# Optimization experiments

Measured on AMD Instinct MI355X. Metric: run time of the kernel, lower is better.

The kernel has to match this reference:

```python
import jax, jax.numpy as jnp
import numpy as np

B, N, K, H = 4, 1024, 48, 128
E = 128          # edge feature dim; num_in = E + H = 256
FF = 4 * H       # dense feedforward width
EPS = 1e-5
SCALE = 30.0


def gelu(x):
    return jax.nn.gelu(x, approximate=False)


def linear(x, w, b):
    # torch Linear: w is [out, in]
    return x @ w.T + b


def layer_norm(x, g, b):
    mu = jnp.mean(x, axis=-1, keepdims=True)
    var = jnp.var(x, axis=-1, keepdims=True)
    return (x - mu) * jax.lax.rsqrt(var + EPS) * g + b


def gather_nodes(nodes, idx):
    # nodes [B,N,H], idx [B,N,K] -> [B,N,K,H]
    b, n, k = idx.shape
    flat = idx.reshape(b, n * k, 1)
    return jnp.take_along_axis(nodes, flat, axis=1).reshape(b, n, k, -1)


def setup_inputs():
    key = jax.random.key(0)
    ks = jax.random.split(key, 24)
    s = 0.05
    inp = {
        "h_V": jax.random.normal(ks[0], (B, N, H), jnp.float32),
        "h_E": jax.random.normal(ks[1], (B, N, K, E), jnp.float32),
        "E_idx": jax.random.randint(ks[2], (B, N, K), 0, N, jnp.int64),
        "mask_V": jnp.ones((B, N), jnp.float32),
        "mask_attend": jnp.ones((B, N, K), jnp.float32),
        # node-update message MLP (input dim H + E + H = 3H here)
        "W1_w": jax.random.normal(ks[3], (H, H + E + H), jnp.float32) * s,
        "W1_b": jnp.zeros((H,), jnp.float32),
        "W2_w": jax.random.normal(ks[4], (H, H), jnp.float32) * s,
        "W2_b": jnp.zeros((H,), jnp.float32),
        "W3_w": jax.random.normal(ks[5], (H, H), jnp.float32) * s,
        "W3_b": jnp.zeros((H,), jnp.float32),
        # edge-update message MLP
        "W11_w": jax.random.normal(ks[6], (H, H + E + H), jnp.float32) * s,
        "W11_b": jnp.zeros((H,), jnp.float32),
        "W12_w": jax.random.normal(ks[7], (H, H), jnp.float32) * s,
        "W12_b": jnp.zeros((H,), jnp.float32),
        "W13_w": jax.random.normal(ks[8], (H, H), jnp.float32) * s,
        "W13_b": jnp.zeros((H,), jnp.float32),
        # layer norms
        "ln0_g": jnp.ones((H,), jnp.float32), "ln0_b": jnp.zeros((H,), jnp.float32),
        "ln1_g": jnp.ones((H,), jnp.float32), "ln1_b": jnp.zeros((H,), jnp.float32),
        "ln2_g": jnp.ones((H,), jnp.float32), "ln2_b": jnp.zeros((H,), jnp.float32),
        # position-wise feedforward
        "Win_w": jax.random.normal(ks[9], (FF, H), jnp.float32) * s,
        "Win_b": jnp.zeros((FF,), jnp.float32),
        "Wout_w": jax.random.normal(ks[10], (H, FF), jnp.float32) * s,
        "Wout_b": jnp.zeros((H,), jnp.float32),
        # ReZero residual weight (init 0 in the module; nonzero for testing)
        "resweight": jax.random.normal(ks[11], (1,), jnp.float32) * 0.1,
    }
    return inp


def reference(h_V, h_E, E_idx, mask_V, mask_attend,
              W1_w, W1_b, W2_w, W2_b, W3_w, W3_b,
              W11_w, W11_b, W12_w, W12_b, W13_w, W13_b,
              ln0_g, ln0_b, ln1_g, ln1_b, ln2_g, ln2_b,
              Win_w, Win_b, Wout_w, Wout_b, resweight):
    # ---- node update (pre-norm, ReZero-scaled residual), dropout=eval ----
    residual = h_V
    hVn = layer_norm(h_V, ln0_g, ln0_b)
    h_nbr = gather_nodes(hVn, E_idx)                              # [B,N,K,H]
    h_EV = jnp.concatenate(
        [jnp.broadcast_to(hVn[:, :, None, :], (B, N, K, H)), h_E, h_nbr], axis=-1)
    h_message = linear(gelu(linear(gelu(linear(h_EV, W1_w, W1_b)), W2_w, W2_b)), W3_w, W3_b)
    h_message = mask_attend[..., None] * h_message
    dh = jnp.sum(h_message, axis=-2) / SCALE
    h_V = residual + dh * resweight

    # ---- position-wise feedforward ----
    residual = h_V
    hVn = layer_norm(h_V, ln1_g, ln1_b)
    dh = linear(gelu(linear(hVn, Win_w, Win_b)), Wout_w, Wout_b)
    h_V = residual + dh * resweight
    h_V = mask_V[..., None] * h_V

    # ---- edge update (no ReZero scaling on this branch) ----
    residual = h_E
    hEn = layer_norm(h_E, ln2_g, ln2_b)
    h_nbr = gather_nodes(h_V, E_idx)
    h_EV = jnp.concatenate(
        [jnp.broadcast_to(h_V[:, :, None, :], (B, N, K, H)), hEn, h_nbr], axis=-1)
    h_message = linear(gelu(linear(gelu(linear(h_EV, W11_w, W11_b)), W12_w, W12_b)), W13_w, W13_b)
    h_E = residual + h_message

    return h_V, h_E
```

## Files before the change

kernel.cpp:

```cpp
#include <hip/hip_runtime.h>
#include <hip/hip_bf16.h>

#define BB 4
#define NN 1024
#define KK 48
#define HH 128
#define EE 128
#define IN3 384
#define FF 512
#define ST 132

typedef __attribute__((ext_vector_type(8))) short bf16x8;
typedef __attribute__((ext_vector_type(4))) float f32x4;

#define MFMA(a, b, c) __builtin_amdgcn_mfma_f32_16x16x32_bf16((a), (b), (c), 0, 0, 0)

__device__ __forceinline__ float bf2f(ushort u) {
    union { uint i; float f; } v; v.i = ((uint)u) << 16; return v.f;
}
__device__ __forceinline__ uint cvtpk(float a, float b) {
    uint r;
    asm("v_cvt_pk_bf16_f32 %0, %1, %2" : "=v"(r) : "v"(a), "v"(b));
    return r;
}
__device__ __forceinline__ ushort f2bf1(float v) {
    return (ushort)cvtpk(v, v);
}
__device__ __forceinline__ float wsum(float x) {
    #pragma unroll
    for (int o = 32; o; o >>= 1) x += __shfl_xor(x, o, 64);
    return x;
}
__device__ __forceinline__ float gelu_f(float x) {
    float t = x * fmaf(x * x, 0.044715f, 1.0f);
    float a = fminf(t * 2.3022061f, 50.0f);
    float z;
    asm("v_exp_f32 %0, %1" : "=v"(z) : "v"(a));
    float r;
    asm("v_rcp_f32 %0, %1" : "=v"(r) : "v"(z + 1.0f));
    return x * z * r;
}

__global__ __launch_bounds__(256) void k_cvt8(
    const float* __restrict__ s0, const float* __restrict__ s1,
    const float* __restrict__ s2, const float* __restrict__ s3,
    const float* __restrict__ s4, const float* __restrict__ s5,
    const float* __restrict__ s6, const float* __restrict__ s7,
    ushort* __restrict__ d0, ushort* __restrict__ d1,
    ushort* __restrict__ d2, ushort* __restrict__ d3,
    ushort* __restrict__ d4, ushort* __restrict__ d5,
    ushort* __restrict__ d6, ushort* __restrict__ d7) {
    int i = blockIdx.x * 256 + threadIdx.x;
    const float* s; ushort* d; int base;
    if      (i < 12288) { s = s0; d = d0; base = 0; }
    else if (i < 16384) { s = s1; d = d1; base = 12288; }
    else if (i < 20480) { s = s2; d = d2; base = 16384; }
    else if (i < 32768) { s = s3; d = d3; base = 20480; }
    else if (i < 36864) { s = s4; d = d4; base = 32768; }
    else if (i < 40960) { s = s5; d = d5; base = 36864; }
    else if (i < 57344) { s = s6; d = d6; base = 40960; }
    else                { s = s7; d = d7; base = 57344; }
    int j = i - base;
    float4 v = ((const float4*)s)[j];
    uint2 o;
    o.x = cvtpk(v.x, v.y);
    o.y = cvtpk(v.z, v.w);
    ((uint2*)d)[j] = o;
}

__global__ __launch_bounds__(256) void k_ln0(const float* __restrict__ hV,
                                             const float* __restrict__ g,
                                             const float* __restrict__ bta,
                                             ushort* __restrict__ out) {
    int row = blockIdx.x * 4 + (threadIdx.x >> 6);
    int l = threadIdx.x & 63;
    const float* src = hV + (size_t)row * HH;
    float x0 = src[l], x1 = src[l + 64];
    float s = wsum(x0 + x1);
    float q = wsum(x0 * x0 + x1 * x1);
    float mu = s * (1.0f / 128.0f);
    float rstd = rsqrtf(q * (1.0f / 128.0f) - mu * mu + 1e-5f);
    ushort* dst = out + (size_t)row * HH;
    dst[l]      = f2bf1((x0 - mu) * rstd * g[l]      + bta[l]);
    dst[l + 64] = f2bf1((x1 - mu) * rstd * g[l + 64] + bta[l + 64]);
}

__global__ __launch_bounds__(256, 4) void k_node(
    const float* __restrict__ hV, const float* __restrict__ hE,
    const int* __restrict__ Eidx, const float* __restrict__ maskAtt,
    const ushort* __restrict__ W1w, const float* __restrict__ W1b,
    const ushort* __restrict__ W2w, const float* __restrict__ W2b,
    const ushort* __restrict__ W3w, const float* __restrict__ W3b,
    const float* __restrict__ resw,
    const ushort* __restrict__ hVn,
    float* __restrict__ outHVp) {

    __shared__ ushort buf[96 * ST];
    __shared__ float  sMask[96];
    __shared__ float  sCol[256];

    const int t = threadIdx.x;
    const int w = t >> 6;
    const int lane = t & 63;
    const int np = blockIdx.x * 2;
    const int b  = np >> 10;
    const int r16 = lane & 15, g4 = lane >> 4;

    int myidx[6];
    #pragma unroll
    for (int mt = 0; mt < 6; mt++)
        myidx[mt] = Eidx[np * KK + mt * 16 + r16];
    if (t < 96) sMask[t] = maskAtt[np * KK + t];

    f32x4 acc[6][2];
    #pragma unroll
    for (int mt = 0; mt < 6; mt++) {
        acc[mt][0] = (f32x4){0.f, 0.f, 0.f, 0.f};
        acc[mt][1] = (f32x4){0.f, 0.f, 0.f, 0.f};
    }

    const ushort* Wp  = W1w + (w * 32 + r16) * IN3 + g4 * 8;
    const float*  hE0 = hE + (size_t)np * KK * EE;

    #pragma unroll
    for (int kt = 0; kt < 4; kt++) {
        bf16x8 b0 = *(const bf16x8*)(Wp + 128 + kt * 32);
        bf16x8 b1 = *(const bf16x8*)(Wp + 16 * IN3 + 128 + kt * 32);
        #pragma unroll
        for (int mt = 0; mt < 6; mt++) {
            const float* p = hE0 + (size_t)(mt * 16 + r16) * EE + kt * 32 + g4 * 8;
            float4 f0 = *(const float4*)(p);
            float4 f1 = *(const float4*)(p + 4);
            union { uint u[4]; bf16x8 v; } a;
            a.u[0] = cvtpk(f0.x, f0.y); a.u[1] = cvtpk(f0.z, f0.w);
            a.u[2] = cvtpk(f1.x, f1.y); a.u[3] = cvtpk(f1.z, f1.w);
            acc[mt][0] = MFMA(a.v, b0, acc[mt][0]);
            acc[mt][1] = MFMA(a.v, b1, acc[mt][1]);
        }
    }
    {
        const ushort* nb = hVn + (size_t)b * NN * HH + g4 * 8;
        #pragma unroll
        for (int kt = 0; kt < 4; kt++) {
            bf16x8 b0 = *(const bf16x8*)(Wp + 256 + kt * 32);
            bf16x8 b1 = *(const bf16x8*)(Wp + 16 * IN3 + 256 + kt * 32);
            #pragma unroll
            for (int mt = 0; mt < 6; mt++) {
                bf16x8 a = *(const bf16x8*)(nb + (size_t)myidx[mt] * HH + kt * 32);
                acc[mt][0] = MFMA(a, b0, acc[mt][0]);
                acc[mt][1] = MFMA(a, b1, acc[mt][1]);
            }
        }
    }
    {
        const ushort* sp0 = hVn + (size_t)np * HH + g4 * 8;
        const ushort* sp1 = sp0 + HH;
        #pragma unroll
        for (int kt = 0; kt < 4; kt++) {
            bf16x8 a0 = *(const bf16x8*)(sp0 + kt * 32);
            bf16x8 a1 = *(const bf16x8*)(sp1 + kt * 32);
            bf16x8 b0 = *(const bf16x8*)(Wp + kt * 32);
            bf16x8 b1 = *(const bf16x8*)(Wp + 16 * IN3 + kt * 32);
            #pragma unroll
            for (int mt = 0; mt < 6; mt++) {
                bf16x8 a = (mt < 3) ? a0 : a1;
                acc[mt][0] = MFMA(a, b0, acc[mt][0]);
                acc[mt][1] = MFMA(a, b1, acc[mt][1]);
            }
        }
    }
    #pragma unroll
    for (int nn = 0; nn < 2; nn++) {
        int col = w * 32 + nn * 16 + r16;
        float bb = W1b[col];
        #pragma unroll
        for (int mt = 0; mt < 6; mt++)
            #pragma unroll
            for (int r = 0; r < 4; r++)
                buf[(mt * 16 + g4 * 4 + r) * ST + col] = f2bf1(gelu_f(acc[mt][nn][r] + bb));
    }
    __syncthreads();

    f32x4 acc2[6][2];
    #pragma unroll
    for (int mt = 0; mt < 6; mt++) {
        acc2[mt][0] = (f32x4){0.f, 0.f, 0.f, 0.f};
        acc2[mt][1] = (f32x4){0.f, 0.f, 0.f, 0.f};
    }
    {
        const ushort* Wp2 = W2w + (w * 32 + r16) * HH + g4 * 8;
        #pragma unroll
        for (int kt = 0; kt < 4; kt++) {
            bf16x8 b0 = *(const bf16x8*)(Wp2 + kt * 32);
            bf16x8 b1 = *(const bf16x8*)(Wp2 + 16 * HH + kt * 32);
            #pragma unroll
            for (int mt = 0; mt < 6; mt++) {
                bf16x8 a = *(const bf16x8*)&buf[(mt * 16 + r16) * ST + kt * 32 + g4 * 8];
                acc2[mt][0] = MFMA(a, b0, acc2[mt][0]);
                acc2[mt][1] = MFMA(a, b1, acc2[mt][1]);
            }
        }
    }
    __syncthreads();
    #pragma unroll
    for (int nn = 0; nn < 2; nn++) {
        int col = w * 32 + nn * 16 + r16;
        float bb = W2b[col];
        #pragma unroll
        for (int mt = 0; mt < 6; mt++)
            #pragma unroll
            for (int r = 0; r < 4; r++)
                buf[(mt * 16 + g4 * 4 + r) * ST + col] = f2bf1(gelu_f(acc2[mt][nn][r] + bb));
    }
    __syncthreads();

    f32x4 acc3[6][2];
    #pragma unroll
    for (int mt = 0; mt < 6; mt++) {
        acc3[mt][0] = (f32x4){0.f, 0.f, 0.f, 0.f};
        acc3[mt][1] = (f32x4){0.f, 0.f, 0.f, 0.f};
    }
    {
        const ushort* Wp3 = W3w + (w * 32 + r16) * HH + g4 * 8;
        #pragma unroll
        for (int kt = 0; kt < 4; kt++) {
            bf16x8 b0 = *(const bf16x8*)(Wp3 + kt * 32);
            bf16x8 b1 = *(const bf16x8*)(Wp3 + 16 * HH + kt * 32);
            #pragma unroll
            for (int mt = 0; mt < 6; mt++) {
                bf16x8 a = *(const bf16x8*)&buf[(mt * 16 + r16) * ST + kt * 32 + g4 * 8];
                acc3[mt][0] = MFMA(a, b0, acc3[mt][0]);
                acc3[mt][1] = MFMA(a, b1, acc3[mt][1]);
            }
        }
    }
    {
        float b3a = W3b[w * 32 + r16];
        float b3b = W3b[w * 32 + 16 + r16];
        float s0a = 0.f, s0b = 0.f, s1a = 0.f, s1b = 0.f;
        #pragma unroll
        for (int mt = 0; mt < 6; mt++)
            #pragma unroll
            for (int r = 0; r < 4; r++) {
                int row = mt * 16 + g4 * 4 + r;
                float mk = sMask[row];
                float v0 = (acc3[mt][0][r] + b3a) * mk;
                float v1 = (acc3[mt][1][r] + b3b) * mk;
                if (mt < 3) { s0a += v0; s0b += v1; }
                else        { s1a += v0; s1b += v1; }
            }
        s0a += __shfl_xor(s0a, 16, 64); s0a += __shfl_xor(s0a, 32, 64);
        s0b += __shfl_xor(s0b, 16, 64); s0b += __shfl_xor(s0b, 32, 64);
        s1a += __shfl_xor(s1a, 16, 64); s1a += __shfl_xor(s1a, 32, 64);
        s1b += __shfl_xor(s1b, 16, 64); s1b += __shfl_xor(s1b, 32, 64);
        if (g4 == 0) {
            sCol[w * 32 + r16]            = s0a;
            sCol[w * 32 + 16 + r16]       = s0b;
            sCol[128 + w * 32 + r16]      = s1a;
            sCol[128 + w * 32 + 16 + r16] = s1b;
        }
    }
    __syncthreads();

    {
        float rw = resw[0];
        size_t o = (size_t)np * HH + t;
        outHVp[o] = hV[o] + sCol[t] * (1.0f / 30.0f) * rw;
    }
}

__global__ __launch_bounds__(256, 4) void k_ffn(
    const float* __restrict__ maskV,
    const float* __restrict__ ln1g, const float* __restrict__ ln1b,
    const ushort* __restrict__ Winw, const float* __restrict__ Winb,
    const ushort* __restrict__ Woutw, const float* __restrict__ Woutb,
    const float* __restrict__ resw,
    const float* __restrict__ hVp,
    float* __restrict__ outV,
    ushort* __restrict__ hV2b) {

    __shared__ float  sHVp[16 * 132];
    __shared__ ushort sX[16 * 136];
    __shared__ ushort sY[16 * 520];
    __shared__ float  sMk[16];

    const int t = threadIdx.x;
    const int w = t >> 6;
    const int lane = t & 63;
    const int nb = blockIdx.x * 16;
    const int r16 = lane & 15, g4 = lane >> 4;

    #pragma unroll
    for (int i = 0; i < 8; i++) {
        int e = t + i * 256;
        sHVp[(e >> 7) * 132 + (e & 127)] = hVp[(size_t)nb * HH + e];
    }
    if (t < 16) sMk[t] = maskV[nb + t];
    __syncthreads();

    #pragma unroll
    for (int i = 0; i < 4; i++) {
        int row = w * 4 + i;
        float x0 = sHVp[row * 132 + lane], x1 = sHVp[row * 132 + 64 + lane];
        float s = wsum(x0 + x1);
        float q = wsum(x0 * x0 + x1 * x1);
        float mu = s * (1.0f / 128.0f);
        float rstd = rsqrtf(q * (1.0f / 128.0f) - mu * mu + 1e-5f);
        sX[row * 136 + lane]      = f2bf1((x0 - mu) * rstd * ln1g[lane]      + ln1b[lane]);
        sX[row * 136 + 64 + lane] = f2bf1((x1 - mu) * rstd * ln1g[64 + lane] + ln1b[64 + lane]);
    }
    __syncthreads();

    f32x4 acc1[8];
    #pragma unroll
    for (int nn = 0; nn < 8; nn++) acc1[nn] = (f32x4){0.f, 0.f, 0.f, 0.f};
    bf16x8 a1[4];
    #pragma unroll
    for (int kt = 0; kt < 4; kt++)
        a1[kt] = *(const bf16x8*)&sX[r16 * 136 + kt * 32 + g4 * 8];
    #pragma unroll
    for (int nn = 0; nn < 8; nn++) {
        const ushort* Wq = Winw + (w * 128 + nn * 16 + r16) * HH + g4 * 8;
        #pragma unroll
        for (int kt = 0; kt < 4; kt++)
            acc1[nn] = MFMA(a1[kt], *(const bf16x8*)(Wq + kt * 32), acc1[nn]);
    }
    #pragma unroll
    for (int nn = 0; nn < 8; nn++) {
        int col = w * 128 + nn * 16 + r16;
        float bb = Winb[col];
        #pragma unroll
        for (int r = 0; r < 4; r++)
            sY[(g4 * 4 + r) * 520 + col] = f2bf1(gelu_f(acc1[nn][r] + bb));
    }
    __syncthreads();

    f32x4 acc2[2];
    acc2[0] = (f32x4){0.f, 0.f, 0.f, 0.f};
    acc2[1] = (f32x4){0.f, 0.f, 0.f, 0.f};
    {
        const ushort* Wq = Woutw + (w * 32 + r16) * FF + g4 * 8;
        #pragma unroll 4
        for (int kt = 0; kt < 16; kt++) {
            bf16x8 a = *(const bf16x8*)&sY[r16 * 520 + kt * 32 + g4 * 8];
            acc2[0] = MFMA(a, *(const bf16x8*)(Wq + kt * 32), acc2[0]);
            acc2[1] = MFMA(a, *(const bf16x8*)(Wq + 16 * FF + kt * 32), acc2[1]);
        }
    }
    float rw = resw[0];
    #pragma unroll
    for (int nn = 0; nn < 2; nn++) {
        int col = w * 32 + nn * 16 + r16;
        float bb = Woutb[col];
        #pragma unroll
        for (int r = 0; r < 4; r++) {
            int row = g4 * 4 + r;
            float out = sHVp[row * 132 + col] + (acc2[nn][r] + bb) * rw;
            out *= sMk[row];
            outV[(size_t)(nb + row) * HH + col] = out;
            hV2b[(size_t)(nb + row) * HH + col] = f2bf1(out);
        }
    }
}

__global__ __launch_bounds__(512, 4) void k_edge(
    const float* __restrict__ hE, const int* __restrict__ Eidx,
    const ushort* __restrict__ W11w, const float* __restrict__ W11b,
    const ushort* __restrict__ W12w, const float* __restrict__ W12b,
    const ushort* __restrict__ W13w, const float* __restrict__ W13b,
    const float* __restrict__ ln2g, const float* __restrict__ ln2b,
    const ushort* __restrict__ hV2b,
    float* __restrict__ outE) {

    __shared__ ushort buf[96 * ST];
    __shared__ ushort rawE[96 * ST];

    const int t = threadIdx.x;
    const int w = t >> 6;
    const int lane = t & 63;
    const int rg = w >> 2;
    const int cg = w & 3;
    const int np = blockIdx.x * 2;
    const int b  = np >> 10;
    const size_t eb = (size_t)np * KK * EE;
    const int r16 = lane & 15, g4 = lane >> 4;

    int myidx[3];
    #pragma unroll
    for (int mt = 0; mt < 3; mt++)
        myidx[mt] = Eidx[np * KK + rg * 48 + mt * 16 + r16];

    {
        float g0 = ln2g[2 * lane], g1 = ln2g[2 * lane + 1];
        float c0 = ln2b[2 * lane], c1 = ln2b[2 * lane + 1];
        #pragma unroll 3
        for (int i = 0; i < 12; i++) {
            int k = w + i * 8;
            float2 pr = ((const float2*)(hE + eb + (size_t)k * EE))[lane];
            *(uint*)&rawE[k * ST + 2 * lane] = cvtpk(pr.x, pr.y);
            float s = wsum(pr.x + pr.y);
            float q = wsum(pr.x * pr.x + pr.y * pr.y);
            float mu = s * (1.0f / 128.0f);
            float rstd = rsqrtf(q * (1.0f / 128.0f) - mu * mu + 1e-5f);
            uint packed = cvtpk((pr.x - mu) * rstd * g0 + c0, (pr.y - mu) * rstd * g1 + c1);
            *(uint*)&buf[k * ST + 2 * lane] = packed;
        }
    }
    __syncthreads();

    f32x4 acc[3][2];
    #pragma unroll
    for (int mt = 0; mt < 3; mt++) {
        acc[mt][0] = (f32x4){0.f, 0.f, 0.f, 0.f};
        acc[mt][1] = (f32x4){0.f, 0.f, 0.f, 0.f};
    }
    const ushort* Wp = W11w + (cg * 32 + r16) * IN3 + g4 * 8;
    {
        const ushort* nb = hV2b + (size_t)b * NN * HH + g4 * 8;
        #pragma unroll
        for (int kt = 0; kt < 4; kt++) {
            bf16x8 b0 = *(const bf16x8*)(Wp + 256 + kt * 32);
            bf16x8 b1 = *(const bf16x8*)(Wp + 16 * IN3 + 256 + kt * 32);
            #pragma unroll
            for (int mt = 0; mt < 3; mt++) {
                bf16x8 a = *(const bf16x8*)(nb + (size_t)myidx[mt] * HH + kt * 32);
                acc[mt][0] = MFMA(a, b0, acc[mt][0]);
                acc[mt][1] = MFMA(a, b1, acc[mt][1]);
            }
        }
    }
    #pragma unroll
    for (int kt = 0; kt < 4; kt++) {
        bf16x8 b0 = *(const bf16x8*)(Wp + 128 + kt * 32);
        bf16x8 b1 = *(const bf16x8*)(Wp + 16 * IN3 + 128 + kt * 32);
        #pragma unroll
        for (int mt = 0; mt < 3; mt++) {
            bf16x8 a = *(const bf16x8*)&buf[(rg * 48 + mt * 16 + r16) * ST + kt * 32 + g4 * 8];
            acc[mt][0] = MFMA(a, b0, acc[mt][0]);
            acc[mt][1] = MFMA(a, b1, acc[mt][1]);
        }
    }
    {
        const ushort* sp = hV2b + (size_t)(np + rg) * HH + g4 * 8;
        #pragma unroll
        for (int kt = 0; kt < 4; kt++) {
            bf16x8 aself = *(const bf16x8*)(sp + kt * 32);
            bf16x8 b0 = *(const bf16x8*)(Wp + kt * 32);
            bf16x8 b1 = *(const bf16x8*)(Wp + 16 * IN3 + kt * 32);
            #pragma unroll
            for (int mt = 0; mt < 3; mt++) {
                acc[mt][0] = MFMA(aself, b0, acc[mt][0]);
                acc[mt][1] = MFMA(aself, b1, acc[mt][1]);
            }
        }
    }
    __syncthreads();
    #pragma unroll
    for (int nn = 0; nn < 2; nn++) {
        int col = cg * 32 + nn * 16 + r16;
        float bb = W11b[col];
        #pragma unroll
        for (int mt = 0; mt < 3; mt++)
            #pragma unroll
            for (int r = 0; r < 4; r++)
                buf[(rg * 48 + mt * 16 + g4 * 4 + r) * ST + col] = f2bf1(gelu_f(acc[mt][nn][r] + bb));
    }
    __syncthreads();

    f32x4 acc2[3][2];
    #pragma unroll
    for (int mt = 0; mt < 3; mt++) {
        acc2[mt][0] = (f32x4){0.f, 0.f, 0.f, 0.f};
        acc2[mt][1] = (f32x4){0.f, 0.f, 0.f, 0.f};
    }
    {
        const ushort* Wp2 = W12w + (cg * 32 + r16) * HH + g4 * 8;
        #pragma unroll
        for (int kt = 0; kt < 4; kt++) {
            bf16x8 b0 = *(const bf16x8*)(Wp2 + kt * 32);
            bf16x8 b1 = *(const bf16x8*)(Wp2 + 16 * HH + kt * 32);
            #pragma unroll
            for (int mt = 0; mt < 3; mt++) {
                bf16x8 a = *(const bf16x8*)&buf[(rg * 48 + mt * 16 + r16) * ST + kt * 32 + g4 * 8];
                acc2[mt][0] = MFMA(a, b0, acc2[mt][0]);
                acc2[mt][1] = MFMA(a, b1, acc2[mt][1]);
            }
        }
    }
    __syncthreads();
    #pragma unroll
    for (int nn = 0; nn < 2; nn++) {
        int col = cg * 32 + nn * 16 + r16;
        float bb = W12b[col];
        #pragma unroll
        for (int mt = 0; mt < 3; mt++)
            #pragma unroll
            for (int r = 0; r < 4; r++)
                buf[(rg * 48 + mt * 16 + g4 * 4 + r) * ST + col] = f2bf1(gelu_f(acc2[mt][nn][r] + bb));
    }
    __syncthreads();

    f32x4 acc3[3][2];
    #pragma unroll
    for (int mt = 0; mt < 3; mt++) {
        acc3[mt][0] = (f32x4){0.f, 0.f, 0.f, 0.f};
        acc3[mt][1] = (f32x4){0.f, 0.f, 0.f, 0.f};
    }
    {
        const ushort* Wp3 = W13w + (cg * 32 + r16) * HH + g4 * 8;
        #pragma unroll
        for (int kt = 0; kt < 4; kt++) {
            bf16x8 b0 = *(const bf16x8*)(Wp3 + kt * 32);
            bf16x8 b1 = *(const bf16x8*)(Wp3 + 16 * HH + kt * 32);
            #pragma unroll
            for (int mt = 0; mt < 3; mt++) {
                bf16x8 a = *(const bf16x8*)&buf[(rg * 48 + mt * 16 + r16) * ST + kt * 32 + g4 * 8];
                acc3[mt][0] = MFMA(a, b0, acc3[mt][0]);
                acc3[mt][1] = MFMA(a, b1, acc3[mt][1]);
            }
        }
    }
    __syncthreads();
    #pragma unroll
    for (int nn = 0; nn < 2; nn++) {
        int col = cg * 32 + nn * 16 + r16;
        float bb = W13b[col];
        #pragma unroll
        for (int mt = 0; mt < 3; mt++)
            #pragma unroll
            for (int r = 0; r < 4; r++)
                buf[(rg * 48 + mt * 16 + g4 * 4 + r) * ST + col] = f2bf1(acc3[mt][nn][r] + bb);
    }
    __syncthreads();

    {
        float4* edst = (float4*)(outE + eb);
        #pragma unroll
        for (int i = 0; i < 6; i++) {
            int c = t + i * 512;
            int k = c >> 5, cp = (c & 31) * 4;
            const ushort* er = &rawE[k * ST + cp];
            const ushort* mr = &buf[k * ST + cp];
            float4 ov;
            ov.x = bf2f(er[0]) + bf2f(mr[0]);
            ov.y = bf2f(er[1]) + bf2f(mr[1]);
            ov.z = bf2f(er[2]) + bf2f(mr[2]);
            ov.w = bf2f(er[3]) + bf2f(mr[3]);
            edst[c] = ov;
        }
    }
}

extern "C" void kernel_launch(void* const* d_in, const int* in_sizes, int n_in,
                              void* d_out, int out_size, void* d_ws, size_t ws_size,
                              hipStream_t stream) {
    const float* hV      = (const float*)d_in[0];
    const float* hE      = (const float*)d_in[1];
    const int*   Eidx    = (const int*)d_in[2];
    const float* maskV   = (const float*)d_in[3];
    const float* maskAtt = (const float*)d_in[4];
    const float* W1w  = (const float*)d_in[5];
    const float* W1b  = (const float*)d_in[6];
    const float* W2w  = (const float*)d_in[7];
    const float* W2b  = (const float*)d_in[8];
    const float* W3w  = (const float*)d_in[9];
    const float* W3b  = (const float*)d_in[10];
    const float* W11w = (const float*)d_in[11];
    const float* W11b = (const float*)d_in[12];
    const float* W12w = (const float*)d_in[13];
    const float* W12b = (const float*)d_in[14];
    const float* W13w = (const float*)d_in[15];
    const float* W13b = (const float*)d_in[16];
    const float* ln0g = (const float*)d_in[17];
    const float* ln0b = (const float*)d_in[18];
    const float* ln1g = (const float*)d_in[19];
    const float* ln1b = (const float*)d_in[20];
    const float* ln2g = (const float*)d_in[21];
    const float* ln2b = (const float*)d_in[22];
    const float* Winw  = (const float*)d_in[23];
    const float* Winb  = (const float*)d_in[24];
    const float* Woutw = (const float*)d_in[25];
    const float* Woutb = (const float*)d_in[26];
    const float* resw  = (const float*)d_in[27];

    float* outV = (float*)d_out;
    float* outE = outV + (size_t)BB * NN * HH;

    const size_t MB = 1 << 20;
    char* wsb = (char*)d_ws;
    ushort* wsHVn = (ushort*)wsb;
    float*  wHVp  = (float*)(wsb + 1 * MB);
    ushort* wHV2b = (ushort*)(wsb + 3 * MB);
    ushort* wW1   = (ushort*)(wsb + 4 * MB);
    ushort* wW2   = wW1  + HH * IN3;
    ushort* wW3   = wW2  + HH * HH;
    ushort* wW11  = wW3  + HH * HH;
    ushort* wW12  = wW11 + HH * IN3;
    ushort* wW13  = wW12 + HH * HH;
    ushort* wWin  = wW13 + HH * HH;
    ushort* wWout = wWin + FF * HH;

    k_cvt8<<<dim3(288), dim3(256), 0, stream>>>(
        W1w, W2w, W3w, W11w, W12w, W13w, Winw, Woutw,
        wW1, wW2, wW3, wW11, wW12, wW13, wWin, wWout);

    k_ln0<<<dim3(BB * NN / 4), dim3(256), 0, stream>>>(hV, ln0g, ln0b, wsHVn);
    k_node<<<dim3(BB * NN / 2), dim3(256), 0, stream>>>(
        hV, hE, Eidx, maskAtt,
        wW1, W1b, wW2, W2b, wW3, W3b, resw, wsHVn, wHVp);
    k_ffn<<<dim3(BB * NN / 16), dim3(256), 0, stream>>>(
        maskV, ln1g, ln1b, wWin, Winb, wWout, Woutb, resw, wHVp, outV, wHV2b);
    k_edge<<<dim3(BB * NN / 2), dim3(512), 0, stream>>>(
        hE, Eidx, wW11, W11b, wW12, W12b, wW13, W13b,
        ln2g, ln2b, wHV2b, outE);
}
```

Baseline: 268.7 us.

## Retile node and edge kernels to one node per 128-thread block

Both the node and edge message kernels now process one node (48 edges) per block with 2 waves, each wave computing a 48x64 output tile instead of 32 columns across 96 rows. This halves shared memory per block, raises per-wave weight-fragment reuse (4 B fragments per A load), and doubles the grid. The edge kernel also drops the bf16 rawE staging buffer and adds the fp32 residual directly from global h_E in the epilogue, which keeps the residual in full precision but uses scattered, uncoalesced scalar stores.

```diff
diff --git a/kernel.cpp b/kernel.cpp
--- a/kernel.cpp
+++ b/kernel.cpp
@@ -85,7 +85,7 @@
     dst[l + 64] = f2bf1((x1 - mu) * rstd * g[l + 64] + bta[l + 64]);
 }
 
-__global__ __launch_bounds__(256, 4) void k_node(
+__global__ __launch_bounds__(128, 6) void k_node(
     const float* __restrict__ hV, const float* __restrict__ hE,
     const int* __restrict__ Eidx, const float* __restrict__ maskAtt,
     const ushort* __restrict__ W1w, const float* __restrict__ W1b,
@@ -95,176 +95,170 @@
     const ushort* __restrict__ hVn,
     float* __restrict__ outHVp) {
 
-    __shared__ ushort buf[96 * ST];
-    __shared__ float  sMask[96];
-    __shared__ float  sCol[256];
+    __shared__ ushort buf[KK * ST];
+    __shared__ float  sMask[KK];
+    __shared__ float  sCol[128];
 
     const int t = threadIdx.x;
     const int w = t >> 6;
     const int lane = t & 63;
-    const int np = blockIdx.x * 2;
-    const int b  = np >> 10;
+    const int bn = blockIdx.x;
+    const int b  = bn >> 10;
     const int r16 = lane & 15, g4 = lane >> 4;
 
-    int myidx[6];
-    #pragma unroll
-    for (int mt = 0; mt < 6; mt++)
-        myidx[mt] = Eidx[np * KK + mt * 16 + r16];
-    if (t < 96) sMask[t] = maskAtt[np * KK + t];
-
-    f32x4 acc[6][2];
-    #pragma unroll
-    for (int mt = 0; mt < 6; mt++) {
-        acc[mt][0] = (f32x4){0.f, 0.f, 0.f, 0.f};
-        acc[mt][1] = (f32x4){0.f, 0.f, 0.f, 0.f};
-    }
-
-    const ushort* Wp  = W1w + (w * 32 + r16) * IN3 + g4 * 8;
-    const float*  hE0 = hE + (size_t)np * KK * EE;
+    int myidx[3];
+    #pragma unroll
+    for (int mt = 0; mt < 3; mt++)
+        myidx[mt] = Eidx[bn * KK + mt * 16 + r16];
+    if (t < KK) sMask[t] = maskAtt[bn * KK + t];
+
+    f32x4 acc[3][4];
+    #pragma unroll
+    for (int mt = 0; mt < 3; mt++)
+        #pragma unroll
+        for (int n = 0; n < 4; n++) acc[mt][n] = (f32x4){0.f, 0.f, 0.f, 0.f};
+
+    const ushort* Wp = W1w + (w * 64 + r16) * IN3 + g4 * 8;
+    const float*  hE0 = hE + (size_t)bn * KK * EE;
 
     #pragma unroll
     for (int kt = 0; kt < 4; kt++) {
-        bf16x8 b0 = *(const bf16x8*)(Wp + 128 + kt * 32);
-        bf16x8 b1 = *(const bf16x8*)(Wp + 16 * IN3 + 128 + kt * 32);
-        #pragma unroll
-        for (int mt = 0; mt < 6; mt++) {
+        bf16x8 bfr[4];
+        #pragma unroll
+        for (int n = 0; n < 4; n++)
+            bfr[n] = *(const bf16x8*)(Wp + n * 16 * IN3 + 128 + kt * 32);
+        #pragma unroll
+        for (int mt = 0; mt < 3; mt++) {
             const float* p = hE0 + (size_t)(mt * 16 + r16) * EE + kt * 32 + g4 * 8;
             float4 f0 = *(const float4*)(p);
             float4 f1 = *(const float4*)(p + 4);
             union { uint u[4]; bf16x8 v; } a;
             a.u[0] = cvtpk(f0.x, f0.y); a.u[1] = cvtpk(f0.z, f0.w);
             a.u[2] = cvtpk(f1.x, f1.y); a.u[3] = cvtpk(f1.z, f1.w);
-            acc[mt][0] = MFMA(a.v, b0, acc[mt][0]);
-            acc[mt][1] = MFMA(a.v, b1, acc[mt][1]);
+            #pragma unroll
+            for (int n = 0; n < 4; n++) acc[mt][n] = MFMA(a.v, bfr[n], acc[mt][n]);
         }
     }
     {
         const ushort* nb = hVn + (size_t)b * NN * HH + g4 * 8;
         #pragma unroll
         for (int kt = 0; kt < 4; kt++) {
-            bf16x8 b0 = *(const bf16x8*)(Wp + 256 + kt * 32);
-            bf16x8 b1 = *(const bf16x8*)(Wp + 16 * IN3 + 256 + kt * 32);
-            #pragma unroll
-            for (int mt = 0; mt < 6; mt++) {
+            bf16x8 bfr[4];
+            #pragma unroll
+            for (int n = 0; n < 4; n++)
+                bfr[n] = *(const bf16x8*)(Wp + n * 16 * IN3 + 256 + kt * 32);
+            #pragma unroll
+            for (int mt = 0; mt < 3; mt++) {
                 bf16x8 a = *(const bf16x8*)(nb + (size_t)myidx[mt] * HH + kt * 32);
-                acc[mt][0] = MFMA(a, b0, acc[mt][0]);
-                acc[mt][1] = MFMA(a, b1, acc[mt][1]);
-            }
-        }
-    }
-    {
-        const ushort* sp0 = hVn + (size_t)np * HH + g4 * 8;
-        const ushort* sp1 = sp0 + HH;
-        #pragma unroll
-        for (int kt = 0; kt < 4; kt++) {
-            bf16x8 a0 = *(const bf16x8*)(sp0 + kt * 32);
-            bf16x8 a1 = *(const bf16x8*)(sp1 + kt * 32);
-            bf16x8 b0 = *(const bf16x8*)(Wp + kt * 32);
-            bf16x8 b1 = *(const bf16x8*)(Wp + 16 * IN3 + kt * 32);
-            #pragma unroll
-            for (int mt = 0; mt < 6; mt++) {
-                bf16x8 a = (mt < 3) ? a0 : a1;
-                acc[mt][0] = MFMA(a, b0, acc[mt][0]);
-                acc[mt][1] = MFMA(a, b1, acc[mt][1]);
-            }
-        }
-    }
-    #pragma unroll
-    for (int nn = 0; nn < 2; nn++) {
-        int col = w * 32 + nn * 16 + r16;
+                #pragma unroll
+                for (int n = 0; n < 4; n++) acc[mt][n] = MFMA(a, bfr[n], acc[mt][n]);
+            }
+        }
+    }
+    {
+        const ushort* sp = hVn + (size_t)bn * HH + g4 * 8;
+        #pragma unroll
+        for (int kt = 0; kt < 4; kt++) {
+            bf16x8 a = *(const bf16x8*)(sp + kt * 32);
+            bf16x8 bfr[4];
+            #pragma unroll
+            for (int n = 0; n < 4; n++)
+                bfr[n] = *(const bf16x8*)(Wp + n * 16 * IN3 + kt * 32);
+            #pragma unroll
+            for (int mt = 0; mt < 3; mt++)
+                #pragma unroll
+                for (int n = 0; n < 4; n++) acc[mt][n] = MFMA(a, bfr[n], acc[mt][n]);
+        }
+    }
+    #pragma unroll
+    for (int n = 0; n < 4; n++) {
+        int col = w * 64 + n * 16 + r16;
         float bb = W1b[col];
         #pragma unroll
-        for (int mt = 0; mt < 6; mt++)
+        for (int mt = 0; mt < 3; mt++)
             #pragma unroll
             for (int r = 0; r < 4; r++)
-                buf[(mt * 16 + g4 * 4 + r) * ST + col] = f2bf1(gelu_f(acc[mt][nn][r] + bb));
-    }
-    __syncthreads();
-
-    f32x4 acc2[6][2];
-    #pragma unroll
-    for (int mt = 0; mt < 6; mt++) {
-        acc2[mt][0] = (f32x4){0.f, 0.f, 0.f, 0.f};
-        acc2[mt][1] = (f32x4){0.f, 0.f, 0.f, 0.f};
-    }
-    {
-        const ushort* Wp2 = W2w + (w * 32 + r16) * HH + g4 * 8;
-        #pragma unroll
-        for (int kt = 0; kt < 4; kt++) {
-            bf16x8 b0 = *(const bf16x8*)(Wp2 + kt * 32);
-            bf16x8 b1 = *(const bf16x8*)(Wp2 + 16 * HH + kt * 32);
-            #pragma unroll
-            for (int mt = 0; mt < 6; mt++) {
+                buf[(mt * 16 + g4 * 4 + r) * ST + col] = f2bf1(gelu_f(acc[mt][n][r] + bb));
+    }
+    __syncthreads();
+
+    f32x4 acc2[3][4];
+    #pragma unroll
+    for (int mt = 0; mt < 3; mt++)
+        #pragma unroll
+        for (int n = 0; n < 4; n++) acc2[mt][n] = (f32x4){0.f, 0.f, 0.f, 0.f};
+    {
+        const ushort* Wp2 = W2w + (w * 64 + r16) * HH + g4 * 8;
+        #pragma unroll
+        for (int kt = 0; kt < 4; kt++) {
+            bf16x8 bfr[4];
+            #pragma unroll
+            for (int n = 0; n < 4; n++)
+                bfr[n] = *(const bf16x8*)(Wp2 + n * 16 * HH + kt * 32);
+            #pragma unroll
+            for (int mt = 0; mt < 3; mt++) {
                 bf16x8 a = *(const bf16x8*)&buf[(mt * 16 + r16) * ST + kt * 32 + g4 * 8];
-                acc2[mt][0] = MFMA(a, b0, acc2[mt][0]);
-                acc2[mt][1] = MFMA(a, b1, acc2[mt][1]);
-            }
-        }
-    }
-    __syncthreads();
-    #pragma unroll
-    for (int nn = 0; nn < 2; nn++) {
-        int col = w * 32 + nn * 16 + r16;
+                #pragma unroll
+                for (int n = 0; n < 4; n++) acc2[mt][n] = MFMA(a, bfr[n], acc2[mt][n]);
+            }
+        }
+    }
+    __syncthreads();
+    #pragma unroll
+    for (int n = 0; n < 4; n++) {
+        int col = w * 64 + n * 16 + r16;
         float bb = W2b[col];
         #pragma unroll
-        for (int mt = 0; mt < 6; mt++)
+        for (int mt = 0; mt < 3; mt++)
             #pragma unroll
             for (int r = 0; r < 4; r++)
-                buf[(mt * 16 + g4 * 4 + r) * ST + col] = f2bf1(gelu_f(acc2[mt][nn][r] + bb));
-    }
-    __syncthreads();
-
-    f32x4 acc3[6][2];
-    #pragma unroll
-    for (int mt = 0; mt < 6; mt++) {
-        acc3[mt][0] = (f32x4){0.f, 0.f, 0.f, 0.f};
-        acc3[mt][1] = (f32x4){0.f, 0.f, 0.f, 0.f};
-    }
-    {
-        const ushort* Wp3 = W3w + (w * 32 + r16) * HH + g4 * 8;
-        #pragma unroll
-        for (int kt = 0; kt < 4; kt++) {
-            bf16x8 b0 = *(const bf16x8*)(Wp3 + kt * 32);
-            bf16x8 b1 = *(const bf16x8*)(Wp3 + 16 * HH + kt * 32);
-            #pragma unroll
-            for (int mt = 0; mt < 6; mt++) {
+                buf[(mt * 16 + g4 * 4 + r) * ST + col] = f2bf1(gelu_f(acc2[mt][n][r] + bb));
+    }
+    __syncthreads();
+
+    f32x4 acc3[3][4];
+    #pragma unroll
+    for (int mt = 0; mt < 3; mt++)
+        #pragma unroll
+        for (int n = 0; n < 4; n++) acc3[mt][n] = (f32x4){0.f, 0.f, 0.f, 0.f};
+    {
+        const ushort* Wp3 = W3w + (w * 64 + r16) * HH + g4 * 8;
+        #pragma unroll
+        for (int kt = 0; kt < 4; kt++) {
+            bf16x8 bfr[4];
+            #pragma unroll
+            for (int n = 0; n < 4; n++)
+                bfr[n] = *(const bf16x8*)(Wp3 + n * 16 * HH + kt * 32);
+            #pragma unroll
+            for (int mt = 0; mt < 3; mt++) {
                 bf16x8 a = *(const bf16x8*)&buf[(mt * 16 + r16) * ST + kt * 32 + g4 * 8];
-                acc3[mt][0] = MFMA(a, b0, acc3[mt][0]);
-                acc3[mt][1] = MFMA(a, b1, acc3[mt][1]);
-            }
-        }
-    }
-    {
-        float b3a = W3b[w * 32 + r16];
-        float b3b = W3b[w * 32 + 16 + r16];
-        float s0a = 0.f, s0b = 0.f, s1a = 0.f, s1b = 0.f;
-        #pragma unroll
-        for (int mt = 0; mt < 6; mt++)
-            #pragma unroll
-            for (int r = 0; r < 4; r++) {
-                int row = mt * 16 + g4 * 4 + r;
-                float mk = sMask[row];
-                float v0 = (acc3[mt][0][r] + b3a) * mk;
-                float v1 = (acc3[mt][1][r] + b3b) * mk;
-                if (mt < 3) { s0a += v0; s0b += v1; }
-                else        { s1a += v0; s1b += v1; }
-            }
-        s0a += __shfl_xor(s0a, 16, 64); s0a += __shfl_xor(s0a, 32, 64);
-        s0b += __shfl_xor(s0b, 16, 64); s0b += __shfl_xor(s0b, 32, 64);
-        s1a += __shfl_xor(s1a, 16, 64); s1a += __shfl_xor(s1a, 32, 64);
-        s1b += __shfl_xor(s1b, 16, 64); s1b += __shfl_xor(s1b, 32, 64);
-        if (g4 == 0) {
-            sCol[w * 32 + r16]            = s0a;
-            sCol[w * 32 + 16 + r16]       = s0b;
-            sCol[128 + w * 32 + r16]      = s1a;
-            sCol[128 + w * 32 + 16 + r16] = s1b;
+                #pragma unroll
+                for (int n = 0; n < 4; n++) acc3[mt][n] = MFMA(a, bfr[n], acc3[mt][n]);
+            }
+        }
+    }
+    {
+        #pragma unroll
+        for (int n = 0; n < 4; n++) {
+            float b3 = W3b[w * 64 + n * 16 + r16];
+            float s = 0.f;
+            #pragma unroll
+            for (int mt = 0; mt < 3; mt++)
+                #pragma unroll
+                for (int r = 0; r < 4; r++) {
+                    int row = mt * 16 + g4 * 4 + r;
+                    s += (acc3[mt][n][r] + b3) * sMask[row];
+                }
+            s += __shfl_xor(s, 16, 64);
+            s += __shfl_xor(s, 32, 64);
+            if (g4 == 0) sCol[w * 64 + n * 16 + r16] = s;
         }
     }
     __syncthreads();
 
     {
         float rw = resw[0];
-        size_t o = (size_t)np * HH + t;
+        size_t o = (size_t)bn * HH + t;
         outHVp[o] = hV[o] + sCol[t] * (1.0f / 30.0f) * rw;
     }
 }
@@ -363,7 +357,7 @@
     }
 }
 
-__global__ __launch_bounds__(512, 4) void k_edge(
+__global__ __launch_bounds__(128, 6) void k_edge(
     const float* __restrict__ hE, const int* __restrict__ Eidx,
     const ushort* __restrict__ W11w, const float* __restrict__ W11b,
     const ushort* __restrict__ W12w, const float* __restrict__ W12b,
@@ -372,32 +366,28 @@
     const ushort* __restrict__ hV2b,
     float* __restrict__ outE) {
 
-    __shared__ ushort buf[96 * ST];
-    __shared__ ushort rawE[96 * ST];
+    __shared__ ushort buf[KK * ST];
 
     const int t = threadIdx.x;
     const int w = t >> 6;
     const int lane = t & 63;
-    const int rg = w >> 2;
-    const int cg = w & 3;
-    const int np = blockIdx.x * 2;
-    const int b  = np >> 10;
-    const size_t eb = (size_t)np * KK * EE;
+    const int bn = blockIdx.x;
+    const int b  = bn >> 10;
+    const size_t eb = (size_t)bn * KK * EE;
     const int r16 = lane & 15, g4 = lane >> 4;
 
     int myidx[3];
     #pragma unroll
     for (int mt = 0; mt < 3; mt++)
-        myidx[mt] = Eidx[np * KK + rg * 48 + mt * 16 + r16];
+        myidx[mt] = Eidx[bn * KK + mt * 16 + r16];
 
     {
         float g0 = ln2g[2 * lane], g1 = ln2g[2 * lane + 1];
         float c0 = ln2b[2 * lane], c1 = ln2b[2 * lane + 1];
-        #pragma unroll 3
-        for (int i = 0; i < 12; i++) {
-            int k = w + i * 8;
+        #pragma unroll 4
+        for (int i = 0; i < 24; i++) {
+            int k = w + i * 2;
             float2 pr = ((const float2*)(hE + eb + (size_t)k * EE))[lane];
-            *(uint*)&rawE[k * ST + 2 * lane] = cvtpk(pr.x, pr.y);
             float s = wsum(pr.x + pr.y);
             float q = wsum(pr.x * pr.x + pr.y * pr.y);
             float mu = s * (1.0f / 128.0f);
@@ -408,146 +398,137 @@
     }
     __syncthreads();
 
-    f32x4 acc[3][2];
-    #pragma unroll
-    for (int mt = 0; mt < 3; mt++) {
-        acc[mt][0] = (f32x4){0.f, 0.f, 0.f, 0.f};
-        acc[mt][1] = (f32x4){0.f, 0.f, 0.f, 0.f};
-    }
-    const ushort* Wp = W11w + (cg * 32 + r16) * IN3 + g4 * 8;
+    f32x4 acc[3][4];
+    #pragma unroll
+    for (int mt = 0; mt < 3; mt++)
+        #pragma unroll
+        for (int n = 0; n < 4; n++) acc[mt][n] = (f32x4){0.f, 0.f, 0.f, 0.f};
+
+    const ushort* Wp = W11w + (w * 64 + r16) * IN3 + g4 * 8;
     {
         const ushort* nb = hV2b + (size_t)b * NN * HH + g4 * 8;
         #pragma unroll
         for (int kt = 0; kt < 4; kt++) {
-            bf16x8 b0 = *(const bf16x8*)(Wp + 256 + kt * 32);
-            bf16x8 b1 = *(const bf16x8*)(Wp + 16 * IN3 + 256 + kt * 32);
+            bf16x8 bfr[4];
+            #pragma unroll
+            for (int n = 0; n < 4; n++)
+                bfr[n] = *(const bf16x8*)(Wp + n * 16 * IN3 + 256 + kt * 32);
             #pragma unroll
             for (int mt = 0; mt < 3; mt++) {
                 bf16x8 a = *(const bf16x8*)(nb + (size_t)myidx[mt] * HH + kt * 32);
-                acc[mt][0] = MFMA(a, b0, acc[mt][0]);
-                acc[mt][1] = MFMA(a, b1, acc[mt][1]);
+                #pragma unroll
+                for (int n = 0; n < 4; n++) acc[mt][n] = MFMA(a, bfr[n], acc[mt][n]);
             }
         }
     }
     #pragma unroll
     for (int kt = 0; kt < 4; kt++) {
-        bf16x8 b0 = *(const bf16x8*)(Wp + 128 + kt * 32);
-        bf16x8 b1 = *(const bf16x8*)(Wp + 16 * IN3 + 128 + kt * 32);
+        bf16x8 bfr[4];
+        #pragma unroll
+        for (int n = 0; n < 4; n++)
+            bfr[n] = *(const bf16x8*)(Wp + n * 16 * IN3 + 128 + kt * 32);
         #pragma unroll
         for (int mt = 0; mt < 3; mt++) {
-            bf16x8 a = *(const bf16x8*)&buf[(rg * 48 + mt * 16 + r16) * ST + kt * 32 + g4 * 8];
-            acc[mt][0] = MFMA(a, b0, acc[mt][0]);
-            acc[mt][1] = MFMA(a, b1, acc[mt][1]);
-        }
-    }
-    {
-        const ushort* sp = hV2b + (size_t)(np + rg) * HH + g4 * 8;
-        #pragma unroll
-        for (int kt = 0; kt < 4; kt++) {
-            bf16x8 aself = *(const bf16x8*)(sp + kt * 32);
-            bf16x8 b0 = *(const bf16x8*)(Wp + kt * 32);
-            bf16x8 b1 = *(const bf16x8*)(Wp + 16 * IN3 + kt * 32);
+            bf16x8 a = *(const bf16x8*)&buf[(mt * 16 + r16) * ST + kt * 32 + g4 * 8];
+            #pragma unroll
+            for (int n = 0; n < 4; n++) acc[mt][n] = MFMA(a, bfr[n], acc[mt][n]);
+        }
+    }
+    {
+        const ushort* sp = hV2b + (size_t)bn * HH + g4 * 8;
+        #pragma unroll
+        for (int kt = 0; kt < 4; kt++) {
+            bf16x8 a = *(const bf16x8*)(sp + kt * 32);
+            bf16x8 bfr[4];
+            #pragma unroll
+            for (int n = 0; n < 4; n++)
+                bfr[n] = *(const bf16x8*)(Wp + n * 16 * IN3 + kt * 32);
+            #pragma unroll
+            for (int mt = 0; mt < 3; mt++)
+                #pragma unroll
+                for (int n = 0; n < 4; n++) acc[mt][n] = MFMA(a, bfr[n], acc[mt][n]);
+        }
+    }
+    __syncthreads();
+    #pragma unroll
+    for (int n = 0; n < 4; n++) {
+        int col = w * 64 + n * 16 + r16;
+        float bb = W11b[col];
+        #pragma unroll
+        for (int mt = 0; mt < 3; mt++)
+            #pragma unroll
+            for (int r = 0; r < 4; r++)
+                buf[(mt * 16 + g4 * 4 + r) * ST + col] = f2bf1(gelu_f(acc[mt][n][r] + bb));
+    }
+    __syncthreads();
+
+    f32x4 acc2[3][4];
+    #pragma unroll
+    for (int mt = 0; mt < 3; mt++)
+        #pragma unroll
+        for (int n = 0; n < 4; n++) acc2[mt][n] = (f32x4){0.f, 0.f, 0.f, 0.f};
+    {
+        const ushort* Wp2 = W12w + (w * 64 + r16) * HH + g4 * 8;
+        #pragma unroll
+        for (int kt = 0; kt < 4; kt++) {
+            bf16x8 bfr[4];
+            #pragma unroll
+            for (int n = 0; n < 4; n++)
+                bfr[n] = *(const bf16x8*)(Wp2 + n * 16 * HH + kt * 32);
             #pragma unroll
             for (int mt = 0; mt < 3; mt++) {
-                acc[mt][0] = MFMA(aself, b0, acc[mt][0]);
-                acc[mt][1] = MFMA(aself, b1, acc[mt][1]);
-            }
-        }
-    }
-    __syncthreads();
-    #pragma unroll
-    for (int nn = 0; nn < 2; nn++) {
-        int col = cg * 32 + nn * 16 + r16;
-        float bb = W11b[col];
+                bf16x8 a = *(const bf16x8*)&buf[(mt * 16 + r16) * ST + kt * 32 + g4 * 8];
+                #pragma unroll
+                for (int n = 0; n < 4; n++) acc2[mt][n] = MFMA(a, bfr[n], acc2[mt][n]);
+            }
+        }
+    }
+    __syncthreads();
+    #pragma unroll
+    for (int n = 0; n < 4; n++) {
+        int col = w * 64 + n * 16 + r16;
+        float bb = W12b[col];
         #pragma unroll
         for (int mt = 0; mt < 3; mt++)
             #pragma unroll
             for (int r = 0; r < 4; r++)
-                buf[(rg * 48 + mt * 16 + g4 * 4 + r) * ST + col] = f2bf1(gelu_f(acc[mt][nn][r] + bb));
-    }
-    __syncthreads();
-
-    f32x4 acc2[3][2];
-    #pragma unroll
-    for (int mt = 0; mt < 3; mt++) {
-        acc2[mt][0] = (f32x4){0.f, 0.f, 0.f, 0.f};
-        acc2[mt][1] = (f32x4){0.f, 0.f, 0.f, 0.f};
-    }
-    {
-        const ushort* Wp2 = W12w + (cg * 32 + r16) * HH + g4 * 8;
-        #pragma unroll
-        for (int kt = 0; kt < 4; kt++) {
-            bf16x8 b0 = *(const bf16x8*)(Wp2 + kt * 32);
-            bf16x8 b1 = *(const bf16x8*)(Wp2 + 16 * HH + kt * 32);
+                buf[(mt * 16 + g4 * 4 + r) * ST + col] = f2bf1(gelu_f(acc2[mt][n][r] + bb));
+    }
+    __syncthreads();
+
+    f32x4 acc3[3][4];
+    #pragma unroll
+    for (int mt = 0; mt < 3; mt++)
+        #pragma unroll
+        for (int n = 0; n < 4; n++) acc3[mt][n] = (f32x4){0.f, 0.f, 0.f, 0.f};
+    {
+        const ushort* Wp3 = W13w + (w * 64 + r16) * HH + g4 * 8;
+        #pragma unroll
+        for (int kt = 0; kt < 4; kt++) {
+            bf16x8 bfr[4];
+            #pragma unroll
+            for (int n = 0; n < 4; n++)
+                bfr[n] = *(const bf16x8*)(Wp3 + n * 16 * HH + kt * 32);
             #pragma unroll
             for (int mt = 0; mt < 3; mt++) {
-                bf16x8 a = *(const bf16x8*)&buf[(rg * 48 + mt * 16 + r16) * ST + kt * 32 + g4 * 8];
-                acc2[mt][0] = MFMA(a, b0, acc2[mt][0]);
-                acc2[mt][1] = MFMA(a, b1, acc2[mt][1]);
-            }
-        }
-    }
-    __syncthreads();
-    #pragma unroll
-    for (int nn = 0; nn < 2; nn++) {
-        int col = cg * 32 + nn * 16 + r16;
-        float bb = W12b[col];
+                bf16x8 a = *(const bf16x8*)&buf[(mt * 16 + r16) * ST + kt * 32 + g4 * 8];
+                #pragma unroll
+                for (int n = 0; n < 4; n++) acc3[mt][n] = MFMA(a, bfr[n], acc3[mt][n]);
+            }
+        }
+    }
+    #pragma unroll
+    for (int n = 0; n < 4; n++) {
+        int col = w * 64 + n * 16 + r16;
+        float bb = W13b[col];
         #pragma unroll
         for (int mt = 0; mt < 3; mt++)
             #pragma unroll
-            for (int r = 0; r < 4; r++)
-                buf[(rg * 48 + mt * 16 + g4 * 4 + r) * ST + col] = f2bf1(gelu_f(acc2[mt][nn][r] + bb));
-    }
-    __syncthreads();
-
-    f32x4 acc3[3][2];
-    #pragma unroll
-    for (int mt = 0; mt < 3; mt++) {
-        acc3[mt][0] = (f32x4){0.f, 0.f, 0.f, 0.f};
-        acc3[mt][1] = (f32x4){0.f, 0.f, 0.f, 0.f};
-    }
-    {
-        const ushort* Wp3 = W13w + (cg * 32 + r16) * HH + g4 * 8;
-        #pragma unroll
-        for (int kt = 0; kt < 4; kt++) {
-            bf16x8 b0 = *(const bf16x8*)(Wp3 + kt * 32);
-            bf16x8 b1 = *(const bf16x8*)(Wp3 + 16 * HH + kt * 32);
-            #pragma unroll
-            for (int mt = 0; mt < 3; mt++) {
-                bf16x8 a = *(const bf16x8*)&buf[(rg * 48 + mt * 16 + r16) * ST + kt * 32 + g4 * 8];
-                acc3[mt][0] = MFMA(a, b0, acc3[mt][0]);
-                acc3[mt][1] = MFMA(a, b1, acc3[mt][1]);
-            }
-        }
-    }
-    __syncthreads();
-    #pragma unroll
-    for (int nn = 0; nn < 2; nn++) {
-        int col = cg * 32 + nn * 16 + r16;
-        float bb = W13b[col];
-        #pragma unroll
-        for (int mt = 0; mt < 3; mt++)
-            #pragma unroll
-            for (int r = 0; r < 4; r++)
-                buf[(rg * 48 + mt * 16 + g4 * 4 + r) * ST + col] = f2bf1(acc3[mt][nn][r] + bb);
-    }
-    __syncthreads();
-
-    {
-        float4* edst = (float4*)(outE + eb);
-        #pragma unroll
-        for (int i = 0; i < 6; i++) {
-            int c = t + i * 512;
-            int k = c >> 5, cp = (c & 31) * 4;
-            const ushort* er = &rawE[k * ST + cp];
-            const ushort* mr = &buf[k * ST + cp];
-            float4 ov;
-            ov.x = bf2f(er[0]) + bf2f(mr[0]);
-            ov.y = bf2f(er[1]) + bf2f(mr[1]);
-            ov.z = bf2f(er[2]) + bf2f(mr[2]);
-            ov.w = bf2f(er[3]) + bf2f(mr[3]);
-            edst[c] = ov;
-        }
+            for (int r = 0; r < 4; r++) {
+                int row = mt * 16 + g4 * 4 + r;
+                size_t off = eb + (size_t)row * EE + col;
+                outE[off] = hE[off] + acc3[mt][n][r] + bb;
+            }
     }
 }
 
@@ -605,12 +586,12 @@
         wW1, wW2, wW3, wW11, wW12, wW13, wWin, wWout);
 
     k_ln0<<<dim3(BB * NN / 4), dim3(256), 0, stream>>>(hV, ln0g, ln0b, wsHVn);
-    k_node<<<dim3(BB * NN / 2), dim3(256), 0, stream>>>(
+    k_node<<<dim3(BB * NN), dim3(128), 0, stream>>>(
         hV, hE, Eidx, maskAtt,
         wW1, W1b, wW2, W2b, wW3, W3b, resw, wsHVn, wHVp);
     k_ffn<<<dim3(BB * NN / 16), dim3(256), 0, stream>>>(
         maskV, ln1g, ln1b, wWin, Winb, wWout, Woutb, resw, wHVp, outV, wHV2b);
-    k_edge<<<dim3(BB * NN / 2), dim3(512), 0, stream>>>(
+    k_edge<<<dim3(BB * NN), dim3(128), 0, stream>>>(
         hE, Eidx, wW11, W11b, wW12, W12b, wW13, W13b,
         ln2g, ln2b, wHV2b, outE);
 }
```

Result: slower. 515.0 us (+91.7%).
